# Kernel optimization log

Measured on AMD Instinct MI355X. Metric: run time of the kernel, lower is better.

## Reference

```python
import jax, jax.numpy as jnp
import numpy as np

N_EMBD = 768
N_HEAD = 12
LN_EPS = 1e-5

def _gelu_tanh(x):
    # 0.5*x*(1+tanh(sqrt(2/pi)*(x+0.044715*x^3)))
    c = 0.7978845608028654
    return 0.5 * x * (1.0 + jnp.tanh(c * (x + 0.044715 * x * x * x)))

def _layernorm(x, g, b):
    mu = jnp.mean(x, axis=-1, keepdims=True)
    var = jnp.mean(jnp.square(x - mu), axis=-1, keepdims=True)
    return (x - mu) * jax.lax.rsqrt(var + LN_EPS) * g + b

def setup_inputs() -> dict:
    key = jax.random.key(0)
    ks = jax.random.split(key, 8)
    C = N_EMBD
    s = 0.02
    return {
        "x": jax.random.normal(ks[0], (4, 2048, C), jnp.float32),
        "ln1_g": jnp.ones((C,), jnp.float32),
        "ln1_b": jnp.zeros((C,), jnp.float32),
        "attn_w": jax.random.normal(ks[1], (3 * C, C), jnp.float32) * s,
        "attn_b": jnp.zeros((3 * C,), jnp.float32),
        "proj_w": jax.random.normal(ks[2], (C, C), jnp.float32) * s,
        "proj_b": jnp.zeros((C,), jnp.float32),
        "ln2_g": jnp.ones((C,), jnp.float32),
        "ln2_b": jnp.zeros((C,), jnp.float32),
        "fc_w": jax.random.normal(ks[3], (4 * C, C), jnp.float32) * s,
        "fc_b": jnp.zeros((4 * C,), jnp.float32),
        "fc2_w": jax.random.normal(ks[4], (C, 4 * C), jnp.float32) * s,
        "fc2_b": jnp.zeros((C,), jnp.float32),
    }

def reference(x, ln1_g, ln1_b, attn_w, attn_b, proj_w, proj_b,
              ln2_g, ln2_b, fc_w, fc_b, fc2_w, fc2_b):
    B, T, C = x.shape
    H = N_HEAD
    D = C // H

    # --- attention branch ---
    h = _layernorm(x, ln1_g, ln1_b)
    qkv = h @ attn_w.T + attn_b            # [B,T,3C]
    q, k, v = jnp.split(qkv, 3, axis=-1)
    q = q.reshape(B, T, H, D).transpose(0, 2, 1, 3)  # [B,H,T,D]
    k = k.reshape(B, T, H, D).transpose(0, 2, 1, 3)
    v = v.reshape(B, T, H, D).transpose(0, 2, 1, 3)

    att = jnp.einsum('bhqd,bhkd->bhqk', q, k) * (1.0 / np.sqrt(D))
    causal = jnp.tril(jnp.ones((T, T), bool))
    att = jnp.where(causal, att, -jnp.inf)
    att = jax.nn.softmax(att, axis=-1)
    y = jnp.einsum('bhqk,bhkd->bhqd', att, v)        # [B,H,T,D]
    y = y.transpose(0, 2, 1, 3).reshape(B, T, C)
    y = y @ proj_w.T + proj_b
    x = x + y

    # --- MLP branch ---
    h2 = _layernorm(x, ln2_g, ln2_b)
    m = _gelu_tanh(h2 @ fc_w.T + fc_b)
    m = m @ fc2_w.T + fc2_b
    return x + m
```

## Files before the change

kernel.cpp:

```cpp
#include <hip/hip_runtime.h>
#include <hip/hip_bf16.h>

#define N_EMBD 768
#define N_HEADS 12
#define HEAD_DIM 64

typedef __attribute__((ext_vector_type(4))) float f32x4;
typedef __attribute__((ext_vector_type(8))) short s16x8;

__device__ __forceinline__ float bf2f(unsigned short u) {
  union { unsigned int i; float f; } z;
  z.i = ((unsigned int)u) << 16;
  return z.f;
}

__device__ __forceinline__ void gload_lds16(const void* g, void* l) {
  __builtin_amdgcn_global_load_lds(
      (const __attribute__((address_space(1))) void*)g,
      (__attribute__((address_space(3))) void*)l, 16, 0, 0);
}

__device__ __forceinline__ float gelu_f(float x) {
  const float c = 0.7978845608028654f;
  float u = c * (x + 0.044715f * x * x * x);
  float t = 1.0f - 2.0f / (__expf(2.0f * u) + 1.0f);
  return 0.5f * x * (1.0f + t);
}

__global__ void cvt4_kernel(const float* __restrict__ s0, __hip_bfloat16* d0,
                            const float* __restrict__ s1, __hip_bfloat16* d1,
                            const float* __restrict__ s2, __hip_bfloat16* d2,
                            const float* __restrict__ s3, __hip_bfloat16* d3,
                            int n0, int n1, int n2, int n3) {
  int i = blockIdx.x * 256 + threadIdx.x;
  if (i < n0) { d0[i] = __float2bfloat16(s0[i]); return; }
  i -= n0;
  if (i < n1) { d1[i] = __float2bfloat16(s1[i]); return; }
  i -= n1;
  if (i < n2) { d2[i] = __float2bfloat16(s2[i]); return; }
  i -= n2;
  if (i < n3) d3[i] = __float2bfloat16(s3[i]);
}

__global__ __launch_bounds__(256) void ln_kernel(
    const float* __restrict__ x, const float* __restrict__ g,
    const float* __restrict__ b, __hip_bfloat16* __restrict__ out) {
  __shared__ float red[8];
  const int row = blockIdx.x;
  const int tid = threadIdx.x;
  const float* xr = x + (size_t)row * N_EMBD;
  float v0 = xr[tid], v1 = xr[tid + 256], v2 = xr[tid + 512];
  float s = v0 + v1 + v2;
#pragma unroll
  for (int m = 32; m >= 1; m >>= 1) s += __shfl_xor(s, m);
  if ((tid & 63) == 0) red[tid >> 6] = s;
  __syncthreads();
  float mu = (red[0] + red[1] + red[2] + red[3]) * (1.0f / 768.0f);
  float d0 = v0 - mu, d1 = v1 - mu, d2 = v2 - mu;
  float ss = d0 * d0 + d1 * d1 + d2 * d2;
  __syncthreads();
#pragma unroll
  for (int m = 32; m >= 1; m >>= 1) ss += __shfl_xor(ss, m);
  if ((tid & 63) == 0) red[4 + (tid >> 6)] = ss;
  __syncthreads();
  float var = (red[4] + red[5] + red[6] + red[7]) * (1.0f / 768.0f);
  float rstd = rsqrtf(var + 1e-5f);
  __hip_bfloat16* orow = out + (size_t)row * N_EMBD;
  orow[tid]       = __float2bfloat16(d0 * rstd * g[tid]       + b[tid]);
  orow[tid + 256] = __float2bfloat16(d1 * rstd * g[tid + 256] + b[tid + 256]);
  orow[tid + 512] = __float2bfloat16(d2 * rstd * g[tid + 512] + b[tid + 512]);
}

#define TILE_M 128
#define TILE_N 128
#define TILE_K 32

template <int EPI>
__global__ __launch_bounds__(256) void gemm_bt(
    const __hip_bfloat16* __restrict__ A, const __hip_bfloat16* __restrict__ W,
    const float* __restrict__ bias, const float* __restrict__ resid,
    __hip_bfloat16* __restrict__ outb, float* __restrict__ outf,
    int M, int N, int K) {
  __shared__ __hip_bfloat16 smA[2][TILE_M * TILE_K];
  __shared__ __hip_bfloat16 smB[2][TILE_N * TILE_K];
  const int tid = threadIdx.x;
  const int lane = tid & 63;
  const int wave = tid >> 6;

  const int nbx = gridDim.x;
  const int nwg = nbx * gridDim.y;
  int bid = blockIdx.y * nbx + blockIdx.x;
  if ((nwg & 7) == 0) bid = (bid & 7) * (nwg >> 3) + (bid >> 3);
  const int m0 = (bid / nbx) * TILE_M;
  const int n0 = (bid % nbx) * TILE_N;
  const int wr = wave >> 1, wc = wave & 1;

  f32x4 acc[4][4];
#pragma unroll
  for (int i = 0; i < 4; ++i)
#pragma unroll
    for (int j = 0; j < 4; ++j) acc[i][j] = f32x4{0.f, 0.f, 0.f, 0.f};

  const int ar0 = tid >> 2;
  const int ac0 = (tid & 3) * 8;
  const __hip_bfloat16* Abase0 = A + (size_t)(m0 + ar0) * K + ac0;
  const __hip_bfloat16* Abase1 = A + (size_t)(m0 + 64 + ar0) * K + ac0;
  const __hip_bfloat16* Wbase0 = W + (size_t)(n0 + ar0) * K + ac0;
  const __hip_bfloat16* Wbase1 = W + (size_t)(n0 + 64 + ar0) * K + ac0;

  auto stage = [&](int buf, int k0) {
    gload_lds16(Abase0 + k0, &smA[buf][wave * 512]);
    gload_lds16(Abase1 + k0, &smA[buf][2048 + wave * 512]);
    gload_lds16(Wbase0 + k0, &smB[buf][wave * 512]);
    gload_lds16(Wbase1 + k0, &smB[buf][2048 + wave * 512]);
  };

  const int rA = lane & 15;
  const int ko = (lane >> 4) * 8;
  const int nk = K / TILE_K;

  stage(0, 0);
  __syncthreads();

  int cur = 0;
  for (int t = 0; t < nk; ++t) {
    if (t + 1 < nk) stage(cur ^ 1, (t + 1) * TILE_K);

    s16x8 af[4], bfr[4];
#pragma unroll
    for (int mi = 0; mi < 4; ++mi)
      af[mi] = *(const s16x8*)&smA[cur][(wr * 64 + mi * 16 + rA) * TILE_K + ko];
#pragma unroll
    for (int ni = 0; ni < 4; ++ni)
      bfr[ni] = *(const s16x8*)&smB[cur][(wc * 64 + ni * 16 + rA) * TILE_K + ko];
#pragma unroll
    for (int mi = 0; mi < 4; ++mi)
#pragma unroll
      for (int ni = 0; ni < 4; ++ni)
        acc[mi][ni] = __builtin_amdgcn_mfma_f32_16x16x32_bf16(
            af[mi], bfr[ni], acc[mi][ni], 0, 0, 0);

    __syncthreads();
    cur ^= 1;
  }

  const int crow = (lane >> 4) * 4;
  const int ccol = lane & 15;
#pragma unroll
  for (int mi = 0; mi < 4; ++mi) {
#pragma unroll
    for (int ni = 0; ni < 4; ++ni) {
      const int col = n0 + wc * 64 + ni * 16 + ccol;
      const float bv = bias[col];
#pragma unroll
      for (int j = 0; j < 4; ++j) {
        const int row = m0 + wr * 64 + mi * 16 + crow + j;
        float v = acc[mi][ni][j] + bv;
        const size_t o = (size_t)row * N + col;
        if (EPI == 0) {
          outb[o] = __float2bfloat16(v);
        } else if (EPI == 1) {
          outb[o] = __float2bfloat16(gelu_f(v));
        } else {
          outf[o] = resid[o] + v;
        }
      }
    }
  }
}

#define AP 72

__global__ __launch_bounds__(256) void attn_mfma(
    const __hip_bfloat16* __restrict__ qkv, __hip_bfloat16* __restrict__ y,
    int T) {
  __shared__ __hip_bfloat16 ks[64 * AP];
  __shared__ __hip_bfloat16 vt[64 * AP];
  __shared__ __hip_bfloat16 ps[4][16 * AP];
  const int tid = threadIdx.x;
  const int lane = tid & 63;
  const int wave = tid >> 6;
  const int b = blockIdx.y / N_HEADS, h = blockIdx.y % N_HEADS;
  const int nq = T / 64;
  const int qa0 = blockIdx.x * 64;
  const int qb0 = (nq - 1 - blockIdx.x) * 64;
  const size_t ldq = 3 * N_EMBD;
  const __hip_bfloat16* qb_ = qkv + (size_t)b * T * ldq + h * HEAD_DIM;
  const __hip_bfloat16* kb = qb_ + N_EMBD;
  const __hip_bfloat16* vb = qb_ + 2 * N_EMBD;

  const int fr = lane & 15;
  const int fo = (lane >> 4) * 8;
  const int crow = (lane >> 4) * 4;

  const float qs = 0.125f * 1.44269504f;
  auto loadq = [&](int qrow, int o) -> s16x8 {
    s16x8 v = *(const s16x8*)(qb_ + (size_t)qrow * ldq + o);
    s16x8 r;
#pragma unroll
    for (int i = 0; i < 8; ++i) {
      float f = bf2f((unsigned short)v[i]) * qs;
      __hip_bfloat16 hb = __float2bfloat16(f);
      r[i] = *reinterpret_cast<short*>(&hb);
    }
    return r;
  };
  s16x8 qfa0 = loadq(qa0 + wave * 16 + fr, fo);
  s16x8 qfa1 = loadq(qa0 + wave * 16 + fr, fo + 32);
  s16x8 qfb0 = loadq(qb0 + wave * 16 + fr, fo);
  s16x8 qfb1 = loadq(qb0 + wave * 16 + fr, fo + 32);

  f32x4 oa[4], ob[4];
  float ma[4], la[4], mb[4], lb_[4];
#pragma unroll
  for (int j = 0; j < 4; ++j) {
    oa[j] = f32x4{0.f, 0.f, 0.f, 0.f};
    ob[j] = f32x4{0.f, 0.f, 0.f, 0.f};
    ma[j] = -1e30f; la[j] = 0.f; mb[j] = -1e30f; lb_[j] = 0.f;
  }

  auto process = [&](const s16x8& q0f, const s16x8& q1f, f32x4 (&o)[4],
                     float (&m_)[4], float (&l_)[4], int tq0, bool diag,
                     int kt) {
    f32x4 sv[4];
#pragma unroll
    for (int sub = 0; sub < 4; ++sub) {
      s16x8 b0 = *(const s16x8*)&ks[(sub * 16 + fr) * AP + fo];
      s16x8 b1 = *(const s16x8*)&ks[(sub * 16 + fr) * AP + 32 + fo];
      f32x4 acc = f32x4{0.f, 0.f, 0.f, 0.f};
      acc = __builtin_amdgcn_mfma_f32_16x16x32_bf16(q0f, b0, acc, 0, 0, 0);
      acc = __builtin_amdgcn_mfma_f32_16x16x32_bf16(q1f, b1, acc, 0, 0, 0);
      sv[sub] = acc;
    }
    if (diag) {
      const int wq0 = tq0 + wave * 16;
#pragma unroll
      for (int sub = 0; sub < 4; ++sub) {
        const int key = kt + sub * 16 + fr;
#pragma unroll
        for (int j = 0; j < 4; ++j)
          if (key > wq0 + crow + j) sv[sub][j] = -1e30f;
      }
    }
    float corr[4];
    bool anyresc = false;
#pragma unroll
    for (int j = 0; j < 4; ++j) {
      float t = fmaxf(fmaxf(sv[0][j], sv[1][j]), fmaxf(sv[2][j], sv[3][j]));
#pragma unroll
      for (int msk = 1; msk <= 8; msk <<= 1) t = fmaxf(t, __shfl_xor(t, msk));
      const bool resc = t > m_[j] + 8.0f;
      corr[j] = resc ? exp2f(m_[j] - t) : 1.0f;
      if (resc) m_[j] = t;
      anyresc = anyresc || resc;
    }
    float rs[4] = {0.f, 0.f, 0.f, 0.f};
#pragma unroll
    for (int sub = 0; sub < 4; ++sub) {
#pragma unroll
      for (int j = 0; j < 4; ++j) {
        float p = exp2f(sv[sub][j] - m_[j]);
        rs[j] += p;
        ps[wave][(crow + j) * AP + sub * 16 + fr] = __float2bfloat16(p);
      }
    }
#pragma unroll
    for (int j = 0; j < 4; ++j) {
#pragma unroll
      for (int msk = 1; msk <= 8; msk <<= 1) rs[j] += __shfl_xor(rs[j], msk);
      l_[j] = l_[j] * corr[j] + rs[j];
    }
    if (__any(anyresc)) {
#pragma unroll
      for (int ds = 0; ds < 4; ++ds)
#pragma unroll
        for (int j = 0; j < 4; ++j) o[ds][j] *= corr[j];
    }
    s16x8 pf0 = *(const s16x8*)&ps[wave][fr * AP + fo];
    s16x8 pf1 = *(const s16x8*)&ps[wave][fr * AP + 32 + fo];
#pragma unroll
    for (int ds = 0; ds < 4; ++ds) {
      s16x8 v0 = *(const s16x8*)&vt[(ds * 16 + fr) * AP + fo];
      s16x8 v1 = *(const s16x8*)&vt[(ds * 16 + fr) * AP + 32 + fo];
      o[ds] = __builtin_amdgcn_mfma_f32_16x16x32_bf16(pf0, v0, o[ds], 0, 0, 0);
      o[ds] = __builtin_amdgcn_mfma_f32_16x16x32_bf16(pf1, v1, o[ds], 0, 0, 0);
    }
  };

  for (int kt = 0; kt <= qb0; kt += 64) {
    __syncthreads();
#pragma unroll
    for (int j = 0; j < 2; ++j) {
      int c = j * 256 + tid;
      int key = c >> 3, d0 = (c & 7) * 8;
      s16x8 kv = *(const s16x8*)(kb + (size_t)(kt + key) * ldq + d0);
      *(s16x8*)&ks[key * AP + d0] = kv;
    }
#pragma unroll
    for (int j = 0; j < 2; ++j) {
      int d0 = (wave * 2 + j) * 8;
      s16x8 vv = *(const s16x8*)(vb + (size_t)(kt + lane) * ldq + d0);
#pragma unroll
      for (int i = 0; i < 8; ++i)
        vt[(d0 + i) * AP + lane] = ((const __hip_bfloat16*)&vv)[i];
    }
    __syncthreads();

    if (kt <= qa0) process(qfa0, qfa1, oa, ma, la, qa0, kt == qa0, kt);
    process(qfb0, qfb1, ob, mb, lb_, qb0, kt == qb0, kt);
  }

#pragma unroll
  for (int j = 0; j < 4; ++j) {
    const float inva = 1.0f / la[j];
    const float invb = 1.0f / lb_[j];
    __hip_bfloat16* ya =
        y + (size_t)(b * T + qa0 + wave * 16 + crow + j) * N_EMBD + h * HEAD_DIM;
    __hip_bfloat16* yb =
        y + (size_t)(b * T + qb0 + wave * 16 + crow + j) * N_EMBD + h * HEAD_DIM;
#pragma unroll
    for (int ds = 0; ds < 4; ++ds) {
      ya[ds * 16 + fr] = __float2bfloat16(oa[ds][j] * inva);
      yb[ds * 16 + fr] = __float2bfloat16(ob[ds][j] * invb);
    }
  }
}

extern "C" void kernel_launch(void* const* d_in, const int* in_sizes, int n_in,
                              void* d_out, int out_size, void* d_ws,
                              size_t ws_size, hipStream_t stream) {
  const int B = 4, T = 2048, C = N_EMBD;
  const int M = B * T;

  const float* x      = (const float*)d_in[0];
  const float* ln1_g  = (const float*)d_in[1];
  const float* ln1_b  = (const float*)d_in[2];
  const float* attn_w = (const float*)d_in[3];
  const float* attn_b = (const float*)d_in[4];
  const float* proj_w = (const float*)d_in[5];
  const float* proj_b = (const float*)d_in[6];
  const float* ln2_g  = (const float*)d_in[7];
  const float* ln2_b  = (const float*)d_in[8];
  const float* fc_w   = (const float*)d_in[9];
  const float* fc_b   = (const float*)d_in[10];
  const float* fc2_w  = (const float*)d_in[11];
  const float* fc2_b  = (const float*)d_in[12];
  float* out = (float*)d_out;

  char* p = (char*)d_ws;
  size_t off = 0;
  auto take = [&](size_t bytes) -> void* {
    void* q = p + off;
    off += (bytes + 1023) & ~(size_t)1023;
    return q;
  };

  __hip_bfloat16* wqkv  = (__hip_bfloat16*)take((size_t)3 * C * C * 2);
  __hip_bfloat16* wproj = (__hip_bfloat16*)take((size_t)C * C * 2);
  __hip_bfloat16* wfc   = (__hip_bfloat16*)take((size_t)4 * C * C * 2);
  __hip_bfloat16* wfc2  = (__hip_bfloat16*)take((size_t)4 * C * C * 2);
  __hip_bfloat16* hbuf  = (__hip_bfloat16*)take((size_t)M * C * 2);
  __hip_bfloat16* big   = (__hip_bfloat16*)take((size_t)M * 4 * C * 2);
  __hip_bfloat16* ybuf  = (__hip_bfloat16*)take((size_t)M * C * 2);
  float*          x1    = (float*)take((size_t)M * C * 4);

  {
    const int n0 = 3 * C * C, n1 = C * C, n2 = 4 * C * C, n3 = 4 * C * C;
    const int ntot = n0 + n1 + n2 + n3;
    cvt4_kernel<<<(ntot + 255) / 256, 256, 0, stream>>>(
        attn_w, wqkv, proj_w, wproj, fc_w, wfc, fc2_w, wfc2, n0, n1, n2, n3);
  }

  ln_kernel<<<M, 256, 0, stream>>>(x, ln1_g, ln1_b, hbuf);
  gemm_bt<0><<<dim3(3 * C / TILE_N, M / TILE_M), 256, 0, stream>>>(
      hbuf, wqkv, attn_b, nullptr, big, nullptr, M, 3 * C, C);
  attn_mfma<<<dim3(T / 128, B * N_HEADS), 256, 0, stream>>>(big, ybuf, T);
  gemm_bt<2><<<dim3(C / TILE_N, M / TILE_M), 256, 0, stream>>>(
      ybuf, wproj, proj_b, x, nullptr, x1, M, C, C);
  ln_kernel<<<M, 256, 0, stream>>>(x1, ln2_g, ln2_b, hbuf);
  gemm_bt<1><<<dim3(4 * C / TILE_N, M / TILE_M), 256, 0, stream>>>(
      hbuf, wfc, fc_b, nullptr, big, nullptr, M, 4 * C, C);
  gemm_bt<2><<<dim3(C / TILE_N, M / TILE_M), 256, 0, stream>>>(
      big, wfc2, fc2_b, x1, nullptr, out, M, C, 4 * C);
}
```

Before: 339.2 us.

## Add 256x128 triple-buffered GEMM kernel for QKV, FC and FC2 projections

```diff
diff --git a/kernel.cpp b/kernel.cpp
--- a/kernel.cpp
+++ b/kernel.cpp
@@ -156,6 +156,158 @@
       for (int j = 0; j < 4; ++j) {
         const int row = m0 + wr * 64 + mi * 16 + crow + j;
         float v = acc[mi][ni][j] + bv;
+        const size_t o = (size_t)row * N + col;
+        if (EPI == 0) {
+          outb[o] = __float2bfloat16(v);
+        } else if (EPI == 1) {
+          outb[o] = __float2bfloat16(gelu_f(v));
+        } else {
+          outf[o] = resid[o] + v;
+        }
+      }
+    }
+  }
+}
+
+#define BM2 256
+#define BN2 128
+#define BK2 64
+
+template <int EPI>
+__global__ __launch_bounds__(512, 2) void gemm256(
+    const __hip_bfloat16* __restrict__ A, const __hip_bfloat16* __restrict__ W,
+    const float* __restrict__ bias, const float* __restrict__ resid,
+    __hip_bfloat16* __restrict__ outb, float* __restrict__ outf,
+    int M, int N, int K) {
+  __shared__ __align__(16) char lds[3][49152];
+  const int tid = threadIdx.x;
+  const int lane = tid & 63;
+  const int wave = tid >> 6;
+  const int wr = wave >> 2;
+  const int wc = wave & 3;
+
+  const int nbx = gridDim.x;
+  const int nwg = nbx * gridDim.y;
+  int bid = blockIdx.y * nbx + blockIdx.x;
+  if ((nwg & 7) == 0) bid = (bid & 7) * (nwg >> 3) + (bid >> 3);
+  const int m0 = (bid / nbx) * BM2;
+  const int n0 = (bid % nbx) * BN2;
+
+  f32x4 acc[8][2];
+#pragma unroll
+  for (int m = 0; m < 8; ++m)
+#pragma unroll
+    for (int n = 0; n < 2; ++n) acc[m][n] = f32x4{0.f, 0.f, 0.f, 0.f};
+
+  auto stage = [&](int slot, int t) {
+    char* base = lds[slot];
+    const int k0 = t * BK2;
+#pragma unroll
+    for (int c = 0; c < 4; ++c) {
+      const int g = c * 512 + tid;
+      const int row = g >> 3;
+      const int col = ((g & 7) ^ (row & 7)) * 8;
+      gload_lds16(A + (size_t)(m0 + row) * K + k0 + col,
+                  base + (c * 512 + wave * 64) * 16);
+    }
+#pragma unroll
+    for (int c = 0; c < 2; ++c) {
+      const int g = c * 512 + tid;
+      const int row = g >> 3;
+      const int col = ((g & 7) ^ (row & 7)) * 8;
+      gload_lds16(W + (size_t)(n0 + row) * K + k0 + col,
+                  base + 32768 + (c * 512 + wave * 64) * 16);
+    }
+  };
+
+  const int fr = lane & 15;
+  const int fq = lane >> 4;
+
+  const int nk = K / BK2;
+  stage(0, 0);
+  if (nk > 1) stage(1 % 3, 1);
+
+  for (int t = 0; t < nk; ++t) {
+    const int slot = t % 3;
+    if (t + 2 < nk) {
+      stage((t + 2) % 3, t + 2);
+      asm volatile("s_waitcnt vmcnt(12)" ::: "memory");
+    } else if (t + 1 < nk) {
+      asm volatile("s_waitcnt vmcnt(6)" ::: "memory");
+    } else {
+      asm volatile("s_waitcnt vmcnt(0)" ::: "memory");
+    }
+    asm volatile("s_barrier" ::: "memory");
+
+    const char* Ab = lds[slot];
+    const char* Bb = lds[slot] + 32768;
+
+    s16x8 bfr[2][2];
+#pragma unroll
+    for (int n = 0; n < 2; ++n)
+#pragma unroll
+      for (int kh = 0; kh < 2; ++kh) {
+        const int row = wc * 32 + n * 16 + fr;
+        const int gc = (kh * 4 + fq) ^ (row & 7);
+        bfr[n][kh] = *(const s16x8*)(Bb + row * 128 + gc * 16);
+      }
+    {
+      s16x8 af[4][2];
+#pragma unroll
+      for (int m = 0; m < 4; ++m)
+#pragma unroll
+        for (int kh = 0; kh < 2; ++kh) {
+          const int row = wr * 128 + m * 16 + fr;
+          const int gc = (kh * 4 + fq) ^ (row & 7);
+          af[m][kh] = *(const s16x8*)(Ab + row * 128 + gc * 16);
+        }
+      __builtin_amdgcn_s_setprio(1);
+#pragma unroll
+      for (int m = 0; m < 4; ++m)
+#pragma unroll
+        for (int n = 0; n < 2; ++n)
+#pragma unroll
+          for (int kh = 0; kh < 2; ++kh)
+            acc[m][n] = __builtin_amdgcn_mfma_f32_16x16x32_bf16(
+                af[m][kh], bfr[n][kh], acc[m][n], 0, 0, 0);
+      __builtin_amdgcn_s_setprio(0);
+    }
+    asm volatile("s_barrier" ::: "memory");
+    {
+      s16x8 ag[4][2];
+#pragma unroll
+      for (int m = 0; m < 4; ++m)
+#pragma unroll
+        for (int kh = 0; kh < 2; ++kh) {
+          const int row = wr * 128 + (m + 4) * 16 + fr;
+          const int gc = (kh * 4 + fq) ^ (row & 7);
+          ag[m][kh] = *(const s16x8*)(Ab + row * 128 + gc * 16);
+        }
+      __builtin_amdgcn_s_setprio(1);
+#pragma unroll
+      for (int m = 0; m < 4; ++m)
+#pragma unroll
+        for (int n = 0; n < 2; ++n)
+#pragma unroll
+          for (int kh = 0; kh < 2; ++kh)
+            acc[m + 4][n] = __builtin_amdgcn_mfma_f32_16x16x32_bf16(
+                ag[m][kh], bfr[n][kh], acc[m + 4][n], 0, 0, 0);
+      __builtin_amdgcn_s_setprio(0);
+    }
+    asm volatile("s_barrier" ::: "memory");
+  }
+
+  const int crow = fq * 4;
+#pragma unroll
+  for (int m = 0; m < 8; ++m) {
+#pragma unroll
+    for (int n = 0; n < 2; ++n) {
+      const int col = n0 + wc * 32 + n * 16 + fr;
+      const float bv = bias[col];
+#pragma unroll
+      for (int j = 0; j < 4; ++j) {
+        const int row = m0 + wr * 128 + m * 16 + crow + j;
+        float v = acc[m][n][j] + bv;
         const size_t o = (size_t)row * N + col;
         if (EPI == 0) {
           outb[o] = __float2bfloat16(v);
@@ -372,14 +524,14 @@
   }
 
   ln_kernel<<<M, 256, 0, stream>>>(x, ln1_g, ln1_b, hbuf);
-  gemm_bt<0><<<dim3(3 * C / TILE_N, M / TILE_M), 256, 0, stream>>>(
+  gemm256<0><<<dim3(3 * C / BN2, M / BM2), 512, 0, stream>>>(
       hbuf, wqkv, attn_b, nullptr, big, nullptr, M, 3 * C, C);
   attn_mfma<<<dim3(T / 128, B * N_HEADS), 256, 0, stream>>>(big, ybuf, T);
   gemm_bt<2><<<dim3(C / TILE_N, M / TILE_M), 256, 0, stream>>>(
       ybuf, wproj, proj_b, x, nullptr, x1, M, C, C);
   ln_kernel<<<M, 256, 0, stream>>>(x1, ln2_g, ln2_b, hbuf);
-  gemm_bt<1><<<dim3(4 * C / TILE_N, M / TILE_M), 256, 0, stream>>>(
+  gemm256<1><<<dim3(4 * C / BN2, M / BM2), 512, 0, stream>>>(
       hbuf, wfc, fc_b, nullptr, big, nullptr, M, 4 * C, C);
-  gemm_bt<2><<<dim3(C / TILE_N, M / TILE_M), 256, 0, stream>>>(
+  gemm256<2><<<dim3(C / BN2, M / BM2), 512, 0, stream>>>(
       big, wfc2, fc2_b, x1, nullptr, out, M, C, 4 * C);
 }
```

New measurement: 340.8 us. Within noise of the previous version (+0.5%).

## Add 256x256 swizzled-LDS GEMM for QKV and FC; single-barrier pipeline in gemm_bt

Applied to the files above, without the earlier changes.

```diff
diff --git a/kernel.cpp b/kernel.cpp
--- a/kernel.cpp
+++ b/kernel.cpp
@@ -120,10 +120,11 @@
   const int nk = K / TILE_K;
 
   stage(0, 0);
-  __syncthreads();
 
   int cur = 0;
   for (int t = 0; t < nk; ++t) {
+    asm volatile("s_waitcnt vmcnt(0)" ::: "memory");
+    asm volatile("s_barrier" ::: "memory");
     if (t + 1 < nk) stage(cur ^ 1, (t + 1) * TILE_K);
 
     s16x8 af[4], bfr[4];
@@ -133,14 +134,14 @@
 #pragma unroll
     for (int ni = 0; ni < 4; ++ni)
       bfr[ni] = *(const s16x8*)&smB[cur][(wc * 64 + ni * 16 + rA) * TILE_K + ko];
+    __builtin_amdgcn_s_setprio(1);
 #pragma unroll
     for (int mi = 0; mi < 4; ++mi)
 #pragma unroll
       for (int ni = 0; ni < 4; ++ni)
         acc[mi][ni] = __builtin_amdgcn_mfma_f32_16x16x32_bf16(
             af[mi], bfr[ni], acc[mi][ni], 0, 0, 0);
-
-    __syncthreads();
+    __builtin_amdgcn_s_setprio(0);
     cur ^= 1;
   }
 
@@ -164,6 +165,122 @@
         } else {
           outf[o] = resid[o] + v;
         }
+      }
+    }
+  }
+}
+
+#define BM3 256
+#define BN3 256
+#define BK3 64
+
+template <int EPI>
+__global__ __launch_bounds__(512, 2) void gemm256b(
+    const __hip_bfloat16* __restrict__ A, const __hip_bfloat16* __restrict__ W,
+    const float* __restrict__ bias,
+    __hip_bfloat16* __restrict__ outb, int M, int N, int K) {
+  __shared__ __align__(16) char lds[2][65536];
+  const int tid = threadIdx.x;
+  const int lane = tid & 63;
+  const int wave = tid >> 6;
+  const int wr = wave >> 2;
+  const int wc = wave & 3;
+
+  const int nbx = gridDim.x;
+  const int nwg = nbx * gridDim.y;
+  int bid = blockIdx.y * nbx + blockIdx.x;
+  if ((nwg & 7) == 0) bid = (bid & 7) * (nwg >> 3) + (bid >> 3);
+  const int m0 = (bid / nbx) * BM3;
+  const int n0 = (bid % nbx) * BN3;
+
+  f32x4 acc[8][4];
+#pragma unroll
+  for (int m = 0; m < 8; ++m)
+#pragma unroll
+    for (int n = 0; n < 4; ++n) acc[m][n] = f32x4{0.f, 0.f, 0.f, 0.f};
+
+  auto stageA = [&](int buf, int t, int c) {
+    const int g = c * 512 + tid;
+    const int row = g >> 3;
+    const int col = ((g & 7) ^ (row & 7)) * 8;
+    gload_lds16(A + (size_t)(m0 + row) * K + t * BK3 + col,
+                lds[buf] + (c * 512 + wave * 64) * 16);
+  };
+  auto stageB = [&](int buf, int t, int c) {
+    const int g = c * 512 + tid;
+    const int row = g >> 3;
+    const int col = ((g & 7) ^ (row & 7)) * 8;
+    gload_lds16(W + (size_t)(n0 + row) * K + t * BK3 + col,
+                lds[buf] + 32768 + (c * 512 + wave * 64) * 16);
+  };
+
+  const int fr = lane & 15;
+  const int fq = lane >> 4;
+  const int nk = K / BK3;
+
+#pragma unroll
+  for (int c = 0; c < 4; ++c) { stageA(0, 0, c); stageB(0, 0, c); }
+
+  int cur = 0;
+  for (int t = 0; t < nk; ++t) {
+    asm volatile("s_waitcnt vmcnt(0)" ::: "memory");
+    asm volatile("s_barrier" ::: "memory");
+    const char* Ab = lds[cur];
+    const char* Bb = lds[cur] + 32768;
+    const bool pre = (t + 1 < nk);
+
+    if (pre) { stageA(cur ^ 1, t + 1, 0); stageB(cur ^ 1, t + 1, 0); }
+
+    s16x8 bfr[4][2];
+#pragma unroll
+    for (int n = 0; n < 4; ++n)
+#pragma unroll
+      for (int kh = 0; kh < 2; ++kh) {
+        const int row = wc * 64 + n * 16 + fr;
+        const int gc = (kh * 4 + fq) ^ (row & 7);
+        bfr[n][kh] = *(const s16x8*)(Bb + row * 128 + gc * 16);
+      }
+
+#pragma unroll
+    for (int p = 0; p < 4; ++p) {
+      if (pre && p > 0) { stageA(cur ^ 1, t + 1, p); stageB(cur ^ 1, t + 1, p); }
+      s16x8 af[2][2];
+#pragma unroll
+      for (int i = 0; i < 2; ++i)
+#pragma unroll
+        for (int kh = 0; kh < 2; ++kh) {
+          const int row = wr * 128 + (2 * p + i) * 16 + fr;
+          const int gc = (kh * 4 + fq) ^ (row & 7);
+          af[i][kh] = *(const s16x8*)(Ab + row * 128 + gc * 16);
+        }
+      __builtin_amdgcn_s_setprio(1);
+#pragma unroll
+      for (int i = 0; i < 2; ++i)
+#pragma unroll
+        for (int n = 0; n < 4; ++n)
+#pragma unroll
+          for (int kh = 0; kh < 2; ++kh)
+            acc[2 * p + i][n] = __builtin_amdgcn_mfma_f32_16x16x32_bf16(
+                af[i][kh], bfr[n][kh], acc[2 * p + i][n], 0, 0, 0);
+      __builtin_amdgcn_s_setprio(0);
+    }
+    cur ^= 1;
+  }
+
+  const int crow = fq * 4;
+#pragma unroll
+  for (int m = 0; m < 8; ++m) {
+#pragma unroll
+    for (int n = 0; n < 4; ++n) {
+      const int col = n0 + wc * 64 + n * 16 + fr;
+      const float bv = bias[col];
+#pragma unroll
+      for (int j = 0; j < 4; ++j) {
+        const int row = m0 + wr * 128 + m * 16 + crow + j;
+        float v = acc[m][n][j] + bv;
+        const size_t o = (size_t)row * N + col;
+        if (EPI == 0) outb[o] = __float2bfloat16(v);
+        else outb[o] = __float2bfloat16(gelu_f(v));
       }
     }
   }
@@ -372,14 +489,14 @@
   }
 
   ln_kernel<<<M, 256, 0, stream>>>(x, ln1_g, ln1_b, hbuf);
-  gemm_bt<0><<<dim3(3 * C / TILE_N, M / TILE_M), 256, 0, stream>>>(
-      hbuf, wqkv, attn_b, nullptr, big, nullptr, M, 3 * C, C);
+  gemm256b<0><<<dim3(3 * C / BN3, M / BM3), 512, 0, stream>>>(
+      hbuf, wqkv, attn_b, big, M, 3 * C, C);
   attn_mfma<<<dim3(T / 128, B * N_HEADS), 256, 0, stream>>>(big, ybuf, T);
   gemm_bt<2><<<dim3(C / TILE_N, M / TILE_M), 256, 0, stream>>>(
       ybuf, wproj, proj_b, x, nullptr, x1, M, C, C);
   ln_kernel<<<M, 256, 0, stream>>>(x1, ln2_g, ln2_b, hbuf);
-  gemm_bt<1><<<dim3(4 * C / TILE_N, M / TILE_M), 256, 0, stream>>>(
-      hbuf, wfc, fc_b, nullptr, big, nullptr, M, 4 * C, C);
+  gemm256b<1><<<dim3(4 * C / BN3, M / BM3), 512, 0, stream>>>(
+      hbuf, wfc, fc_b, big, M, 4 * C, C);
   gemm_bt<2><<<dim3(C / TILE_N, M / TILE_M), 256, 0, stream>>>(
       big, wfc2, fc2_b, x1, nullptr, out, M, C, 4 * C);
 }
```

Result: no change. 345.9 us (+2.0%).

## Double-buffer attention K/V tiles and transpose S layout; single barrier in GEMM loop

Applied to the files above, without the earlier changes.

```diff
diff --git a/kernel.cpp b/kernel.cpp
--- a/kernel.cpp
+++ b/kernel.cpp
@@ -120,10 +120,11 @@
   const int nk = K / TILE_K;
 
   stage(0, 0);
-  __syncthreads();
 
   int cur = 0;
   for (int t = 0; t < nk; ++t) {
+    asm volatile("s_waitcnt vmcnt(0)" ::: "memory");
+    asm volatile("s_barrier" ::: "memory");
     if (t + 1 < nk) stage(cur ^ 1, (t + 1) * TILE_K);
 
     s16x8 af[4], bfr[4];
@@ -133,14 +134,14 @@
 #pragma unroll
     for (int ni = 0; ni < 4; ++ni)
       bfr[ni] = *(const s16x8*)&smB[cur][(wc * 64 + ni * 16 + rA) * TILE_K + ko];
+    __builtin_amdgcn_s_setprio(1);
 #pragma unroll
     for (int mi = 0; mi < 4; ++mi)
 #pragma unroll
       for (int ni = 0; ni < 4; ++ni)
         acc[mi][ni] = __builtin_amdgcn_mfma_f32_16x16x32_bf16(
             af[mi], bfr[ni], acc[mi][ni], 0, 0, 0);
-
-    __syncthreads();
+    __builtin_amdgcn_s_setprio(0);
     cur ^= 1;
   }
 
@@ -174,8 +175,8 @@
 __global__ __launch_bounds__(256) void attn_mfma(
     const __hip_bfloat16* __restrict__ qkv, __hip_bfloat16* __restrict__ y,
     int T) {
-  __shared__ __hip_bfloat16 ks[64 * AP];
-  __shared__ __hip_bfloat16 vt[64 * AP];
+  __shared__ __hip_bfloat16 ks[2][64 * AP];
+  __shared__ __hip_bfloat16 vt[2][64 * AP];
   __shared__ __hip_bfloat16 ps[4][16 * AP];
   const int tid = threadIdx.x;
   const int lane = tid & 63;
@@ -211,109 +212,119 @@
   s16x8 qfb1 = loadq(qb0 + wave * 16 + fr, fo + 32);
 
   f32x4 oa[4], ob[4];
-  float ma[4], la[4], mb[4], lb_[4];
 #pragma unroll
   for (int j = 0; j < 4; ++j) {
     oa[j] = f32x4{0.f, 0.f, 0.f, 0.f};
     ob[j] = f32x4{0.f, 0.f, 0.f, 0.f};
-    ma[j] = -1e30f; la[j] = 0.f; mb[j] = -1e30f; lb_[j] = 0.f;
-  }
-
-  auto process = [&](const s16x8& q0f, const s16x8& q1f, f32x4 (&o)[4],
-                     float (&m_)[4], float (&l_)[4], int tq0, bool diag,
+  }
+  float m_a = -1e30f, l_a = 0.f, m_b = -1e30f, l_b = 0.f;
+
+  s16x8 kr0, kr1, vr0, vr1;
+  const int krow0 = tid >> 3;
+  const int kcol = (tid & 7) * 8;
+  const int vkey = 2 * (lane & 31);
+  const int vd0 = wave * 16 + (lane >> 5) * 8;
+
+  auto loadKV = [&](int kt) {
+    kr0 = *(const s16x8*)(kb + (size_t)(kt + krow0) * ldq + kcol);
+    kr1 = *(const s16x8*)(kb + (size_t)(kt + 32 + krow0) * ldq + kcol);
+    vr0 = *(const s16x8*)(vb + (size_t)(kt + vkey) * ldq + vd0);
+    vr1 = *(const s16x8*)(vb + (size_t)(kt + vkey + 1) * ldq + vd0);
+  };
+  auto writeKV = [&](int bufi) {
+    *(s16x8*)&ks[bufi][krow0 * AP + kcol] = kr0;
+    *(s16x8*)&ks[bufi][(32 + krow0) * AP + kcol] = kr1;
+#pragma unroll
+    for (int i = 0; i < 8; ++i) {
+      unsigned u = (unsigned short)vr0[i] | ((unsigned)(unsigned short)vr1[i] << 16);
+      *(unsigned*)&vt[bufi][(vd0 + i) * AP + vkey] = u;
+    }
+  };
+
+  auto process = [&](int bufi, const s16x8& q0f, const s16x8& q1f,
+                     f32x4 (&o)[4], float& m_, float& l_, int tq0, bool diag,
                      int kt) {
     f32x4 sv[4];
 #pragma unroll
     for (int sub = 0; sub < 4; ++sub) {
-      s16x8 b0 = *(const s16x8*)&ks[(sub * 16 + fr) * AP + fo];
-      s16x8 b1 = *(const s16x8*)&ks[(sub * 16 + fr) * AP + 32 + fo];
+      s16x8 k0 = *(const s16x8*)&ks[bufi][(sub * 16 + fr) * AP + fo];
+      s16x8 k1 = *(const s16x8*)&ks[bufi][(sub * 16 + fr) * AP + 32 + fo];
       f32x4 acc = f32x4{0.f, 0.f, 0.f, 0.f};
-      acc = __builtin_amdgcn_mfma_f32_16x16x32_bf16(q0f, b0, acc, 0, 0, 0);
-      acc = __builtin_amdgcn_mfma_f32_16x16x32_bf16(q1f, b1, acc, 0, 0, 0);
+      acc = __builtin_amdgcn_mfma_f32_16x16x32_bf16(k0, q0f, acc, 0, 0, 0);
+      acc = __builtin_amdgcn_mfma_f32_16x16x32_bf16(k1, q1f, acc, 0, 0, 0);
       sv[sub] = acc;
     }
+    const int qg = tq0 + wave * 16 + fr;
     if (diag) {
-      const int wq0 = tq0 + wave * 16;
-#pragma unroll
-      for (int sub = 0; sub < 4; ++sub) {
-        const int key = kt + sub * 16 + fr;
+#pragma unroll
+      for (int sub = 0; sub < 4; ++sub)
 #pragma unroll
         for (int j = 0; j < 4; ++j)
-          if (key > wq0 + crow + j) sv[sub][j] = -1e30f;
+          if (kt + sub * 16 + crow + j > qg) sv[sub][j] = -1e30f;
+    }
+    float t = fmaxf(fmaxf(sv[0][0], sv[0][1]), fmaxf(sv[0][2], sv[0][3]));
+#pragma unroll
+    for (int sub = 1; sub < 4; ++sub)
+      t = fmaxf(t, fmaxf(fmaxf(sv[sub][0], sv[sub][1]),
+                         fmaxf(sv[sub][2], sv[sub][3])));
+    t = fmaxf(t, __shfl_xor(t, 16));
+    t = fmaxf(t, __shfl_xor(t, 32));
+    const bool resc = t > m_ + 8.0f;
+    const float corr = resc ? exp2f(m_ - t) : 1.0f;
+    if (resc) m_ = t;
+    float rs = 0.f;
+#pragma unroll
+    for (int sub = 0; sub < 4; ++sub) {
+#pragma unroll
+      for (int j = 0; j < 4; ++j) {
+        float p = exp2f(sv[sub][j] - m_);
+        rs += p;
+        ps[wave][fr * AP + sub * 16 + crow + j] = __float2bfloat16(p);
       }
     }
-    float corr[4];
-    bool anyresc = false;
-#pragma unroll
-    for (int j = 0; j < 4; ++j) {
-      float t = fmaxf(fmaxf(sv[0][j], sv[1][j]), fmaxf(sv[2][j], sv[3][j]));
-#pragma unroll
-      for (int msk = 1; msk <= 8; msk <<= 1) t = fmaxf(t, __shfl_xor(t, msk));
-      const bool resc = t > m_[j] + 8.0f;
-      corr[j] = resc ? exp2f(m_[j] - t) : 1.0f;
-      if (resc) m_[j] = t;
-      anyresc = anyresc || resc;
-    }
-    float rs[4] = {0.f, 0.f, 0.f, 0.f};
-#pragma unroll
-    for (int sub = 0; sub < 4; ++sub) {
+    rs += __shfl_xor(rs, 16);
+    rs += __shfl_xor(rs, 32);
+    l_ = l_ * corr + rs;
+    if (__any(resc)) {
 #pragma unroll
       for (int j = 0; j < 4; ++j) {
-        float p = exp2f(sv[sub][j] - m_[j]);
-        rs[j] += p;
-        ps[wave][(crow + j) * AP + sub * 16 + fr] = __float2bfloat16(p);
+        const float cj = __shfl(corr, (lane & 0x30) | (crow + j));
+#pragma unroll
+        for (int ds = 0; ds < 4; ++ds) o[ds][j] *= cj;
       }
-    }
-#pragma unroll
-    for (int j = 0; j < 4; ++j) {
-#pragma unroll
-      for (int msk = 1; msk <= 8; msk <<= 1) rs[j] += __shfl_xor(rs[j], msk);
-      l_[j] = l_[j] * corr[j] + rs[j];
-    }
-    if (__any(anyresc)) {
-#pragma unroll
-      for (int ds = 0; ds < 4; ++ds)
-#pragma unroll
-        for (int j = 0; j < 4; ++j) o[ds][j] *= corr[j];
     }
     s16x8 pf0 = *(const s16x8*)&ps[wave][fr * AP + fo];
     s16x8 pf1 = *(const s16x8*)&ps[wave][fr * AP + 32 + fo];
 #pragma unroll
     for (int ds = 0; ds < 4; ++ds) {
-      s16x8 v0 = *(const s16x8*)&vt[(ds * 16 + fr) * AP + fo];
-      s16x8 v1 = *(const s16x8*)&vt[(ds * 16 + fr) * AP + 32 + fo];
+      s16x8 v0 = *(const s16x8*)&vt[bufi][(ds * 16 + fr) * AP + fo];
+      s16x8 v1 = *(const s16x8*)&vt[bufi][(ds * 16 + fr) * AP + 32 + fo];
       o[ds] = __builtin_amdgcn_mfma_f32_16x16x32_bf16(pf0, v0, o[ds], 0, 0, 0);
       o[ds] = __builtin_amdgcn_mfma_f32_16x16x32_bf16(pf1, v1, o[ds], 0, 0, 0);
     }
   };
 
+  loadKV(0);
+  writeKV(0);
+  __syncthreads();
+  int cur = 0;
   for (int kt = 0; kt <= qb0; kt += 64) {
+    const bool hasnext = (kt + 64 <= qb0);
+    if (hasnext) loadKV(kt + 64);
+    if (kt <= qa0)
+      process(cur, qfa0, qfa1, oa, m_a, l_a, qa0, kt == qa0, kt);
+    process(cur, qfb0, qfb1, ob, m_b, l_b, qb0, kt == qb0, kt);
+    if (hasnext) writeKV(cur ^ 1);
     __syncthreads();
-#pragma unroll
-    for (int j = 0; j < 2; ++j) {
-      int c = j * 256 + tid;
-      int key = c >> 3, d0 = (c & 7) * 8;
-      s16x8 kv = *(const s16x8*)(kb + (size_t)(kt + key) * ldq + d0);
-      *(s16x8*)&ks[key * AP + d0] = kv;
-    }
-#pragma unroll
-    for (int j = 0; j < 2; ++j) {
-      int d0 = (wave * 2 + j) * 8;
-      s16x8 vv = *(const s16x8*)(vb + (size_t)(kt + lane) * ldq + d0);
-#pragma unroll
-      for (int i = 0; i < 8; ++i)
-        vt[(d0 + i) * AP + lane] = ((const __hip_bfloat16*)&vv)[i];
-    }
-    __syncthreads();
-
-    if (kt <= qa0) process(qfa0, qfa1, oa, ma, la, qa0, kt == qa0, kt);
-    process(qfb0, qfb1, ob, mb, lb_, qb0, kt == qb0, kt);
+    cur ^= 1;
   }
 
 #pragma unroll
   for (int j = 0; j < 4; ++j) {
-    const float inva = 1.0f / la[j];
-    const float invb = 1.0f / lb_[j];
+    const float la_j = __shfl(l_a, (lane & 0x30) | (crow + j));
+    const float lb_j = __shfl(l_b, (lane & 0x30) | (crow + j));
+    const float inva = 1.0f / la_j;
+    const float invb = 1.0f / lb_j;
     __hip_bfloat16* ya =
         y + (size_t)(b * T + qa0 + wave * 16 + crow + j) * N_EMBD + h * HEAD_DIM;
     __hip_bfloat16* yb =
```

Result: faster. 300.2 us (-11.5%).
